# Performance work log

Measured on AMD Instinct MI355X. Metric: run time of the kernel, lower is better.

Reference implementation:

```python
import jax, jax.numpy as jnp
import numpy as np

N_INNER = 2000  # number of inner tree nodes, divisible by 5 (gen_A grouping)
N_LEAF = 10000  # vocabulary / leaf count
N_DOC = 128     # number of documents


def _build_inv_A(n_inner):
    """Static structural matrix: A_full = I - [0 | A], inverted once (host-side numpy)."""
    m = n_inner // 5
    A = np.zeros((n_inner, n_inner - 1), dtype=np.float32)
    for r in range(m - 1):
        A[r, 5 * r:5 * r + 5] = 1.0
    A[m - 1, 5 * (m - 1):] = 1.0
    A_full = np.eye(n_inner, dtype=np.float32) - np.concatenate(
        [np.zeros((n_inner, 1), dtype=np.float32), A], axis=1)
    return jnp.asarray(np.linalg.inv(A_full))


def setup_inputs() -> dict:
    key = jax.random.key(0)
    k1, k2 = jax.random.split(key)
    mass = jax.random.uniform(k1, (N_DOC, N_LEAF), dtype=jnp.float32)
    mass = mass / mass.sum(axis=1, keepdims=True)  # probability mass per doc
    param = jax.random.normal(k2, (N_INNER, N_LEAF), dtype=jnp.float32)
    return {"mass": mass, "param": param}


def reference(mass, param):
    n_inner = param.shape[0]
    inv_A = _build_inv_A(n_inner)               # (n_inner, n_inner), static
    sm = jax.nn.softmax(param, axis=0)
    # hard column-wise argmax one-hot, as in calc_psub (ge of column max)
    B = (sm >= sm.max(axis=0, keepdims=True)).astype(mass.dtype)
    psub = inv_A @ B                            # (n_inner, n_leaf) subtree indicator
    # distance[i,j] = |psub @ (m_i - m_j)|_1 + |m_i - m_j|_1
    # = pairwise L1 on concatenated features [mass @ psub.T, mass]
    proj = mass @ psub.T                        # (n_doc, n_inner)
    feat = jnp.concatenate([proj, mass], axis=1)  # (n_doc, n_inner + n_leaf)
    return jnp.abs(feat[:, None, :] - feat[None, :, :]).sum(-1)  # (n_doc, n_doc)
```

## Files before the change

### kernel.cpp

```cpp
#include <hip/hip_runtime.h>

#define N_INNER 2000
#define N_LEAF  10000
#define N_DOC   128
#define AM_CHUNKS 50
#define AM_ROWS   40
#define DW   64
#define DCH  188

__device__ __forceinline__ unsigned enc_f32(float f) {
    unsigned u = __float_as_uint(f);
    return (u & 0x80000000u) ? ~u : (u | 0x80000000u);
}

__global__ __launch_bounds__(256) void k_amax(const float* __restrict__ param,
                                              unsigned long long* __restrict__ packed) {
    int j0 = (blockIdx.x * 256 + threadIdx.x) * 4;
    if (j0 >= N_LEAF) return;
    int r0 = blockIdx.y * AM_ROWS;
    float b0 = -1e30f, b1 = -1e30f, b2 = -1e30f, b3 = -1e30f;
    unsigned i0 = 0, i1 = 0, i2 = 0, i3 = 0;
    const float* p = param + (size_t)r0 * N_LEAF + j0;
    #pragma unroll 8
    for (int r = 0; r < AM_ROWS; ++r) {
        float4 v = *(const float4*)p;
        p += N_LEAF;
        unsigned row = (unsigned)(r0 + r);
        if (v.x > b0) { b0 = v.x; i0 = row; }
        if (v.y > b1) { b1 = v.y; i1 = row; }
        if (v.z > b2) { b2 = v.z; i2 = row; }
        if (v.w > b3) { b3 = v.w; i3 = row; }
    }
    atomicMax(&packed[j0 + 0], ((unsigned long long)enc_f32(b0) << 32) | i0);
    atomicMax(&packed[j0 + 1], ((unsigned long long)enc_f32(b1) << 32) | i1);
    atomicMax(&packed[j0 + 2], ((unsigned long long)enc_f32(b2) << 32) | i2);
    atomicMax(&packed[j0 + 3], ((unsigned long long)enc_f32(b3) << 32) | i3);
}

__global__ __launch_bounds__(256) void k_wscan_proj(const unsigned long long* __restrict__ packed,
                                                    const float* __restrict__ mass,
                                                    float* __restrict__ proj,
                                                    float* __restrict__ S) {
    __shared__ float wl[N_INNER];
    __shared__ float Px[N_INNER + 1];
    __shared__ float wsum[4], wsum2[4];
    int d = blockIdx.x, t = threadIdx.x;
    for (int k = t; k < N_INNER; k += 256) wl[k] = 0.f;
    __syncthreads();
    const float* md = mass + (size_t)d * N_LEAF;
    const unsigned* pw = (const unsigned*)packed;
    #pragma unroll
    for (int it = 0; it < 10; ++it) {
        int j0 = (t + it * 256) * 4;
        if (j0 < N_LEAF) {
            float4 v = *(const float4*)(md + j0);
            atomicAdd(&wl[pw[2 * (j0 + 0)]], v.x);
            atomicAdd(&wl[pw[2 * (j0 + 1)]], v.y);
            atomicAdd(&wl[pw[2 * (j0 + 2)]], v.z);
            atomicAdd(&wl[pw[2 * (j0 + 3)]], v.w);
        }
    }
    __syncthreads();
    float loc[8];
    float s = 0.f, s2 = 0.f;
    #pragma unroll
    for (int k = 0; k < 8; ++k) {
        int idx = t * 8 + k;
        float v = (idx < N_INNER) ? wl[idx] : 0.f;
        loc[k] = s;
        s += v;
        float dep = (float)((idx >= 1) + (idx >= 6) + (idx >= 31) + (idx >= 156) + (idx >= 781) + 2);
        s2 += dep * v;
    }
    int lane = t & 63, w = t >> 6;
    float ws = s;
    #pragma unroll
    for (int off = 1; off < 64; off <<= 1) {
        float o = __shfl_up(ws, off, 64);
        if (lane >= off) ws += o;
    }
    float r2 = s2;
    #pragma unroll
    for (int off = 32; off > 0; off >>= 1) r2 += __shfl_down(r2, off, 64);
    if (lane == 63) wsum[w] = ws;
    if (lane == 0)  wsum2[w] = r2;
    __syncthreads();
    float base = ws - s;
    for (int q = 0; q < w; ++q) base += wsum[q];
    #pragma unroll
    for (int k = 0; k < 8; ++k) {
        int idx = t * 8 + k;
        if (idx <= N_INNER) Px[idx] = base + loc[k];
    }
    if (t == 0) S[d] = (wsum2[0] + wsum2[1]) + (wsum2[2] + wsum2[3]);
    __syncthreads();
    float* pd = proj + (size_t)d * N_INNER;
    #pragma unroll
    for (int k = 0; k < 8; ++k) {
        int i = t + k * 256;
        if (i < N_INNER) {
            float sum = 0.f;
            int s0 = i, e0 = i;
            while (s0 < N_INNER) {
                int ee = (e0 < N_INNER - 1) ? e0 : (N_INNER - 1);
                sum += Px[ee + 1] - Px[s0];
                s0 = 5 * s0 + 1;
                e0 = 5 * e0 + 5;
            }
            pd[i] = sum;
        }
    }
}

__global__ __launch_bounds__(256) void k_dist(const float* __restrict__ proj,
                                              const float* __restrict__ mass,
                                              float* __restrict__ partial) {
    __shared__ float lds[192 * DW];
    int t = threadIdx.x;
    int ch = blockIdx.x, jt = blockIdx.y;
    int c0 = ch * DW;
    int jbase = jt * 64;
    #pragma unroll
    for (int k = 0; k < 12; ++k) {
        int f = t + k * 256;
        int row = f >> 4, g = f & 15;
        int doc = (row < 128) ? row : (jbase + (row - 128));
        int col = c0 + g * 4;
        float4 v = make_float4(0.f, 0.f, 0.f, 0.f);
        if (col < N_INNER)               v = *(const float4*)(proj + (size_t)doc * N_INNER + col);
        else if (col < N_INNER + N_LEAF) v = *(const float4*)(mass + (size_t)doc * N_LEAF + (col - N_INNER));
        int gg = g ^ ((row >> 3) & 7);
        *(float4*)(&lds[row * DW + gg * 4]) = v;
    }
    __syncthreads();
    int tx = t & 15, ty = t >> 4;
    int ib = ty * 8;
    int jb = 128 + tx * 4;
    int swi = ty & 7;
    int swj = (tx >> 1) & 7;
    float acc[8][4];
    #pragma unroll
    for (int r = 0; r < 8; ++r)
        #pragma unroll
        for (int q = 0; q < 4; ++q) acc[r][q] = 0.f;
    #pragma unroll 4
    for (int cg = 0; cg < 16; ++cg) {
        float4 bv[4];
        #pragma unroll
        for (int jr = 0; jr < 4; ++jr)
            bv[jr] = *(const float4*)(&lds[(jb + jr) * DW + ((cg ^ swj) << 2)]);
        #pragma unroll
        for (int r = 0; r < 8; ++r) {
            float4 av = *(const float4*)(&lds[(ib + r) * DW + ((cg ^ swi) << 2)]);
            #pragma unroll
            for (int q = 0; q < 4; ++q) {
                acc[r][q] += (fminf(av.x, bv[q].x) + fminf(av.y, bv[q].y))
                           + (fminf(av.z, bv[q].z) + fminf(av.w, bv[q].w));
            }
        }
    }
    float* pp = partial + (size_t)ch * 16384 + jbase;
    #pragma unroll
    for (int r = 0; r < 8; ++r) {
        *(float4*)(pp + (size_t)(ib + r) * 128 + tx * 4) =
            make_float4(acc[r][0], acc[r][1], acc[r][2], acc[r][3]);
    }
}

__global__ __launch_bounds__(256) void k_out(const float* __restrict__ partial,
                                             const float* __restrict__ S,
                                             float* __restrict__ out) {
    int p = blockIdx.x * 256 + threadIdx.x;
    float s0 = 0.f, s1 = 0.f, s2 = 0.f, s3 = 0.f;
    #pragma unroll 8
    for (int c = 0; c < DCH; c += 4) {
        s0 += partial[(size_t)(c + 0) * 16384 + p];
        s1 += partial[(size_t)(c + 1) * 16384 + p];
        s2 += partial[(size_t)(c + 2) * 16384 + p];
        s3 += partial[(size_t)(c + 3) * 16384 + p];
    }
    int i = p >> 7, j = p & 127;
    out[p] = S[i] + S[j] - 2.f * ((s0 + s1) + (s2 + s3));
}

extern "C" void kernel_launch(void* const* d_in, const int* in_sizes, int n_in,
                              void* d_out, int out_size, void* d_ws, size_t ws_size,
                              hipStream_t stream) {
    const float* mass  = (const float*)d_in[0];
    const float* param = (const float*)d_in[1];
    float* out = (float*)d_out;
    char* ws = (char*)d_ws;

    unsigned long long* packed = (unsigned long long*)(ws + 0);
    float* proj    = (float*)(ws + 80000);
    float* S       = (float*)(ws + 1104000);
    float* partial = (float*)(ws + 1104512);

    hipMemsetAsync(packed, 0, N_LEAF * sizeof(unsigned long long), stream);
    k_amax       <<<dim3(10, AM_CHUNKS), 256, 0, stream>>>(param, packed);
    k_wscan_proj <<<dim3(N_DOC),         256, 0, stream>>>(packed, mass, proj, S);
    k_dist       <<<dim3(DCH, 2),        256, 0, stream>>>(proj, mass, partial);
    k_out        <<<dim3(64),            256, 0, stream>>>(partial, S, out);
}
```

Measured before the change: 175.4 us.

## Fuse all stages into persistent megakernel with grid barriers and overlapped mass tiles

Replaces four kernel launches with one persistent kernel of 376 blocks that synchronise through atomic grid barriers. While some blocks run the column argmax over param, the others compute the mass-only part of the pairwise min-sum, since that part does not depend on the argmax. The proj-dependent columns are then done in a later phase with smaller 32-wide tiles, and the partial reductions are split across two phases. This removes launch gaps and hides the argmax behind the distance work. In exchange it depends on every block being co-resident for the spin barriers, and it adds barrier latency.

```diff
diff --git a/kernel.cpp b/kernel.cpp
--- a/kernel.cpp
+++ b/kernel.cpp
@@ -3,26 +3,48 @@
 #define N_INNER 2000
 #define N_LEAF  10000
 #define N_DOC   128
-#define AM_CHUNKS 50
-#define AM_ROWS   40
-#define DW   64
-#define DCH  188
+
+#define NBLK  376
+#define AMAXB 250
+#define MCH   156
+#define PCH   63
+
+#define WS_BAR     0
+#define WS_PACKED  128
+#define WS_PROJ    81920
+#define WS_S       1105920
+#define WS_PART    1106432
+#define WS_MRED    9363968
 
 __device__ __forceinline__ unsigned enc_f32(float f) {
     unsigned u = __float_as_uint(f);
     return (u & 0x80000000u) ? ~u : (u | 0x80000000u);
 }
 
-__global__ __launch_bounds__(256) void k_amax(const float* __restrict__ param,
-                                              unsigned long long* __restrict__ packed) {
-    int j0 = (blockIdx.x * 256 + threadIdx.x) * 4;
+__device__ __forceinline__ void grid_bar(unsigned* cnt, unsigned target) {
+    __syncthreads();
+    if (threadIdx.x == 0) {
+        __threadfence();
+        __hip_atomic_fetch_add(cnt, 1u, __ATOMIC_ACQ_REL, __HIP_MEMORY_SCOPE_AGENT);
+        while (__hip_atomic_load(cnt, __ATOMIC_ACQUIRE, __HIP_MEMORY_SCOPE_AGENT) < target)
+            __builtin_amdgcn_s_sleep(2);
+        __threadfence();
+    }
+    __syncthreads();
+}
+
+__device__ __forceinline__ void amax_unit(const float* __restrict__ param,
+                                          unsigned long long* __restrict__ packed,
+                                          int u, int t) {
+    int stripe = u / 50, rc = u % 50;
+    int j0 = (stripe * 256 + t) * 4;
     if (j0 >= N_LEAF) return;
-    int r0 = blockIdx.y * AM_ROWS;
+    int r0 = rc * 40;
     float b0 = -1e30f, b1 = -1e30f, b2 = -1e30f, b3 = -1e30f;
     unsigned i0 = 0, i1 = 0, i2 = 0, i3 = 0;
     const float* p = param + (size_t)r0 * N_LEAF + j0;
     #pragma unroll 8
-    for (int r = 0; r < AM_ROWS; ++r) {
+    for (int r = 0; r < 40; ++r) {
         float4 v = *(const float4*)p;
         p += N_LEAF;
         unsigned row = (unsigned)(r0 + r);
@@ -37,14 +59,101 @@
     atomicMax(&packed[j0 + 3], ((unsigned long long)enc_f32(b3) << 32) | i3);
 }
 
-__global__ __launch_bounds__(256) void k_wscan_proj(const unsigned long long* __restrict__ packed,
-                                                    const float* __restrict__ mass,
-                                                    float* __restrict__ proj,
-                                                    float* __restrict__ S) {
-    __shared__ float wl[N_INNER];
-    __shared__ float Px[N_INNER + 1];
-    __shared__ float wsum[4], wsum2[4];
-    int d = blockIdx.x, t = threadIdx.x;
+__device__ __forceinline__ void mass_tile_acc(const float* __restrict__ mass,
+                                              float* lds, int c, int jbase, int t,
+                                              float acc[8][4]) {
+    int mc0 = 16 + c * 64;
+    __syncthreads();
+    #pragma unroll
+    for (int k = 0; k < 12; ++k) {
+        int f = t + k * 256;
+        int row = f >> 4, g = f & 15;
+        int doc = (row < 128) ? row : (jbase + (row - 128));
+        float4 v = *(const float4*)(mass + (size_t)doc * N_LEAF + mc0 + g * 4);
+        int gg = g ^ ((row >> 3) & 7);
+        *(float4*)(&lds[row * 64 + gg * 4]) = v;
+    }
+    __syncthreads();
+    int tx = t & 15, ty = t >> 4;
+    int ib = ty * 8;
+    int jb = 128 + tx * 4;
+    int swi = ty & 7;
+    int swj = (tx >> 1) & 7;
+    #pragma unroll 4
+    for (int cgi = 0; cgi < 16; ++cgi) {
+        float4 bv[4];
+        #pragma unroll
+        for (int jr = 0; jr < 4; ++jr)
+            bv[jr] = *(const float4*)(&lds[(jb + jr) * 64 + ((cgi ^ swj) << 2)]);
+        #pragma unroll
+        for (int r = 0; r < 8; ++r) {
+            float4 av = *(const float4*)(&lds[(ib + r) * 64 + ((cgi ^ swi) << 2)]);
+            #pragma unroll
+            for (int q = 0; q < 4; ++q) {
+                acc[r][q] += (fminf(av.x, bv[q].x) + fminf(av.y, bv[q].y))
+                           + (fminf(av.z, bv[q].z) + fminf(av.w, bv[q].w));
+            }
+        }
+    }
+}
+
+__device__ __forceinline__ void proj_tile(const float* __restrict__ proj,
+                                          const float* __restrict__ mass,
+                                          float* __restrict__ partial,
+                                          float* lds, int c, int jbase, int t) {
+    int f0 = c * 32;
+    __syncthreads();
+    #pragma unroll
+    for (int k = 0; k < 6; ++k) {
+        int f = t + k * 256;
+        int row = f >> 3, g = f & 7;
+        int doc = (row < 128) ? row : (jbase + (row - 128));
+        int col = f0 + g * 4;
+        float4 v;
+        if (col < N_INNER) v = *(const float4*)(proj + (size_t)doc * N_INNER + col);
+        else               v = *(const float4*)(mass + (size_t)doc * N_LEAF + (col - N_INNER));
+        int gg = g ^ ((row >> 2) & 7);
+        *(float4*)(&lds[row * 32 + gg * 4]) = v;
+    }
+    __syncthreads();
+    int tx = t & 15, ty = t >> 4;
+    int ib = ty * 8;
+    int jb = 128 + tx * 4;
+    int swj = tx & 7;
+    float acc[8][4] = {};
+    #pragma unroll
+    for (int cgi = 0; cgi < 8; ++cgi) {
+        float4 bv[4];
+        #pragma unroll
+        for (int jr = 0; jr < 4; ++jr)
+            bv[jr] = *(const float4*)(&lds[(jb + jr) * 32 + ((cgi ^ swj) << 2)]);
+        #pragma unroll
+        for (int r = 0; r < 8; ++r) {
+            int swi = ((ib + r) >> 2) & 7;
+            float4 av = *(const float4*)(&lds[(ib + r) * 32 + ((cgi ^ swi) << 2)]);
+            #pragma unroll
+            for (int q = 0; q < 4; ++q) {
+                acc[r][q] += (fminf(av.x, bv[q].x) + fminf(av.y, bv[q].y))
+                           + (fminf(av.z, bv[q].z) + fminf(av.w, bv[q].w));
+            }
+        }
+    }
+    float* pp = partial + (size_t)(PCH + c) * 16384 + jbase;
+    #pragma unroll
+    for (int r = 0; r < 8; ++r)
+        *(float4*)(pp + (size_t)(ib + r) * 128 + tx * 4) =
+            make_float4(acc[r][0], acc[r][1], acc[r][2], acc[r][3]);
+}
+
+__device__ __forceinline__ void wscan_body(const unsigned long long* __restrict__ packed,
+                                           const float* __restrict__ mass,
+                                           float* __restrict__ proj,
+                                           float* __restrict__ S,
+                                           char* smem, int d, int t) {
+    float* wl = (float*)smem;
+    float* Px = wl + N_INNER;
+    float* wsum  = Px + N_INNER + 1;
+    float* wsum2 = wsum + 4;
     for (int k = t; k < N_INNER; k += 256) wl[k] = 0.f;
     __syncthreads();
     const float* md = mass + (size_t)d * N_LEAF;
@@ -112,75 +221,78 @@
     }
 }
 
-__global__ __launch_bounds__(256) void k_dist(const float* __restrict__ proj,
-                                              const float* __restrict__ mass,
-                                              float* __restrict__ partial) {
-    __shared__ float lds[192 * DW];
-    int t = threadIdx.x;
-    int ch = blockIdx.x, jt = blockIdx.y;
-    int c0 = ch * DW;
-    int jbase = jt * 64;
-    #pragma unroll
-    for (int k = 0; k < 12; ++k) {
-        int f = t + k * 256;
-        int row = f >> 4, g = f & 15;
-        int doc = (row < 128) ? row : (jbase + (row - 128));
-        int col = c0 + g * 4;
-        float4 v = make_float4(0.f, 0.f, 0.f, 0.f);
-        if (col < N_INNER)               v = *(const float4*)(proj + (size_t)doc * N_INNER + col);
-        else if (col < N_INNER + N_LEAF) v = *(const float4*)(mass + (size_t)doc * N_LEAF + (col - N_INNER));
-        int gg = g ^ ((row >> 3) & 7);
-        *(float4*)(&lds[row * DW + gg * 4]) = v;
-    }
-    __syncthreads();
-    int tx = t & 15, ty = t >> 4;
-    int ib = ty * 8;
-    int jb = 128 + tx * 4;
-    int swi = ty & 7;
-    int swj = (tx >> 1) & 7;
-    float acc[8][4];
-    #pragma unroll
-    for (int r = 0; r < 8; ++r)
-        #pragma unroll
-        for (int q = 0; q < 4; ++q) acc[r][q] = 0.f;
-    #pragma unroll 4
-    for (int cg = 0; cg < 16; ++cg) {
-        float4 bv[4];
-        #pragma unroll
-        for (int jr = 0; jr < 4; ++jr)
-            bv[jr] = *(const float4*)(&lds[(jb + jr) * DW + ((cg ^ swj) << 2)]);
-        #pragma unroll
-        for (int r = 0; r < 8; ++r) {
-            float4 av = *(const float4*)(&lds[(ib + r) * DW + ((cg ^ swi) << 2)]);
-            #pragma unroll
-            for (int q = 0; q < 4; ++q) {
-                acc[r][q] += (fminf(av.x, bv[q].x) + fminf(av.y, bv[q].y))
-                           + (fminf(av.z, bv[q].z) + fminf(av.w, bv[q].w));
-            }
-        }
-    }
-    float* pp = partial + (size_t)ch * 16384 + jbase;
-    #pragma unroll
-    for (int r = 0; r < 8; ++r) {
-        *(float4*)(pp + (size_t)(ib + r) * 128 + tx * 4) =
-            make_float4(acc[r][0], acc[r][1], acc[r][2], acc[r][3]);
-    }
-}
-
-__global__ __launch_bounds__(256) void k_out(const float* __restrict__ partial,
-                                             const float* __restrict__ S,
-                                             float* __restrict__ out) {
-    int p = blockIdx.x * 256 + threadIdx.x;
-    float s0 = 0.f, s1 = 0.f, s2 = 0.f, s3 = 0.f;
-    #pragma unroll 8
-    for (int c = 0; c < DCH; c += 4) {
-        s0 += partial[(size_t)(c + 0) * 16384 + p];
-        s1 += partial[(size_t)(c + 1) * 16384 + p];
-        s2 += partial[(size_t)(c + 2) * 16384 + p];
-        s3 += partial[(size_t)(c + 3) * 16384 + p];
-    }
-    int i = p >> 7, j = p & 127;
-    out[p] = S[i] + S[j] - 2.f * ((s0 + s1) + (s2 + s3));
+__global__ __launch_bounds__(256, 2) void mega(const float* __restrict__ mass,
+                                               const float* __restrict__ param,
+                                               float* __restrict__ out,
+                                               unsigned* __restrict__ bar,
+                                               unsigned long long* __restrict__ packed,
+                                               float* __restrict__ proj,
+                                               float* __restrict__ S,
+                                               float* __restrict__ partial,
+                                               float* __restrict__ mred) {
+    __shared__ __align__(16) char smem[49152];
+    float* lds = (float*)smem;
+    int bid = blockIdx.x, t = threadIdx.x;
+
+    if (bid < AMAXB) {
+        for (int u = bid; u < 500; u += AMAXB)
+            amax_unit(param, packed, u, t);
+    } else {
+        int b = bid - AMAXB;
+        int jbase = (b & 1) * 64;
+        int q = b >> 1;
+        float acc[8][4] = {};
+        #pragma unroll 1
+        for (int k = 0; k < 3; ++k) {
+            int c = q + 63 * k;
+            if (c >= MCH) break;
+            mass_tile_acc(mass, lds, c, jbase, t, acc);
+        }
+        int tx = t & 15, ty = t >> 4;
+        float* pp = partial + (size_t)q * 16384 + jbase;
+        #pragma unroll
+        for (int r = 0; r < 8; ++r)
+            *(float4*)(pp + (size_t)(ty * 8 + r) * 128 + tx * 4) =
+                make_float4(acc[r][0], acc[r][1], acc[r][2], acc[r][3]);
+    }
+    grid_bar(bar, NBLK);
+
+    if (bid < N_DOC) {
+        wscan_body(packed, mass, proj, S, smem, bid, t);
+    } else if (bid < N_DOC + 64) {
+        int p = (bid - N_DOC) * 256 + t;
+        float s0 = 0.f, s1 = 0.f, s2 = 0.f, s3 = 0.f;
+        int c = 0;
+        for (; c + 4 <= 63; c += 4) {
+            s0 += partial[(size_t)(c + 0) * 16384 + p];
+            s1 += partial[(size_t)(c + 1) * 16384 + p];
+            s2 += partial[(size_t)(c + 2) * 16384 + p];
+            s3 += partial[(size_t)(c + 3) * 16384 + p];
+        }
+        for (; c < 63; ++c) s0 += partial[(size_t)c * 16384 + p];
+        mred[p] = (s0 + s1) + (s2 + s3);
+    }
+    grid_bar(bar, 2 * NBLK);
+
+    if (bid < 2 * PCH) {
+        proj_tile(proj, mass, partial, lds, bid >> 1, (bid & 1) * 64, t);
+    }
+    grid_bar(bar, 3 * NBLK);
+
+    if (bid < 64) {
+        int p = bid * 256 + t;
+        float s0 = mred[p], s1 = 0.f, s2 = 0.f, s3 = 0.f;
+        int c = 0;
+        for (; c + 4 <= PCH; c += 4) {
+            s0 += partial[(size_t)(PCH + c + 0) * 16384 + p];
+            s1 += partial[(size_t)(PCH + c + 1) * 16384 + p];
+            s2 += partial[(size_t)(PCH + c + 2) * 16384 + p];
+            s3 += partial[(size_t)(PCH + c + 3) * 16384 + p];
+        }
+        for (; c < PCH; ++c) s0 += partial[(size_t)(PCH + c) * 16384 + p];
+        int i = p >> 7, j = p & 127;
+        out[p] = S[i] + S[j] - 2.f * ((s0 + s1) + (s2 + s3));
+    }
 }
 
 extern "C" void kernel_launch(void* const* d_in, const int* in_sizes, int n_in,
@@ -191,14 +303,14 @@
     float* out = (float*)d_out;
     char* ws = (char*)d_ws;
 
-    unsigned long long* packed = (unsigned long long*)(ws + 0);
-    float* proj    = (float*)(ws + 80000);
-    float* S       = (float*)(ws + 1104000);
-    float* partial = (float*)(ws + 1104512);
-
-    hipMemsetAsync(packed, 0, N_LEAF * sizeof(unsigned long long), stream);
-    k_amax       <<<dim3(10, AM_CHUNKS), 256, 0, stream>>>(param, packed);
-    k_wscan_proj <<<dim3(N_DOC),         256, 0, stream>>>(packed, mass, proj, S);
-    k_dist       <<<dim3(DCH, 2),        256, 0, stream>>>(proj, mass, partial);
-    k_out        <<<dim3(64),            256, 0, stream>>>(partial, S, out);
-}
+    unsigned*           bar     = (unsigned*)(ws + WS_BAR);
+    unsigned long long* packed  = (unsigned long long*)(ws + WS_PACKED);
+    float*              proj    = (float*)(ws + WS_PROJ);
+    float*              S       = (float*)(ws + WS_S);
+    float*              partial = (float*)(ws + WS_PART);
+    float*              mred    = (float*)(ws + WS_MRED);
+
+    hipMemsetAsync(ws, 0, WS_PACKED + N_LEAF * sizeof(unsigned long long), stream);
+    mega<<<dim3(NBLK), dim3(256), 0, stream>>>(mass, param, out, bar, packed,
+                                               proj, S, partial, mred);
+}
```

New measurement: 410.9 us. +134.3%, slower.
